# Performance work log

Measured on AMD Instinct MI355X. Metric: run time of the kernel, lower is better.

Reference implementation:

```python
import jax, jax.numpy as jnp
import numpy as np

N_NODES = 50000
N_EDGES = 800000
IN_DIM = 256
HID_DIM = 512
OUT_DIM = 256


def setup_inputs() -> dict:
    key = jax.random.key(0)
    ks = jax.random.split(key, 8)
    x = jax.random.normal(ks[0], (N_NODES, IN_DIM), dtype=jnp.float32)
    src = jax.random.randint(ks[1], (N_EDGES,), 0, N_NODES, dtype=jnp.int32)
    dst = jax.random.randint(ks[2], (N_EDGES,), 0, N_NODES, dtype=jnp.int32)
    s = 1.0 / np.sqrt(IN_DIM)
    W_self = jax.random.uniform(ks[3], (IN_DIM, HID_DIM), jnp.float32, -s, s)
    W_neigh = jax.random.uniform(ks[4], (IN_DIM, HID_DIM), jnp.float32, -s, s)
    b_enc = jnp.zeros((HID_DIM,), jnp.float32)
    s2 = 1.0 / np.sqrt(HID_DIM)
    W_dec = jax.random.uniform(ks[5], (HID_DIM, OUT_DIM), jnp.float32, -s2, s2)
    b_dec = jax.random.uniform(ks[6], (OUT_DIM,), jnp.float32, -s2, s2)
    return {"x": x, "src": src, "dst": dst, "W_self": W_self,
            "W_neigh": W_neigh, "b_enc": b_enc, "W_dec": W_dec, "b_dec": b_dec}


def reference(x, src, dst, W_self, W_neigh, b_enc, W_dec, b_dec):
    n = x.shape[0]
    # mean neighbor aggregation: scatter-sum src features onto dst, divide by in-degree
    deg = jax.ops.segment_sum(jnp.ones(dst.shape, x.dtype), dst, num_segments=n)
    neigh_sum = jax.ops.segment_sum(x[src], dst, num_segments=n)  # [N, in_dim]
    neigh_mean = neigh_sum / jnp.clip(deg, 1.0)[:, None]
    # SAGEConv 'mean': fc_self(x) + fc_neigh(h_neigh) + bias, then relu
    h = jax.nn.relu(x @ W_self + neigh_mean @ W_neigh + b_enc)  # [N, hid]
    reconstructed = h @ W_dec + b_dec  # [N, out]
    return (reconstructed, h)
```

## Files before the change

kernel.cpp:

```cpp
#include <hip/hip_runtime.h>
#include <stdint.h>

#define N_NODES 50000
#define N_EDGES 800000
#define IN_DIM 256
#define HID_DIM 512
#define OUT_DIM 256
#define SCAN_BLOCKS 196

__device__ __forceinline__ uint16_t f2b(float f) {
    uint32_t u = __builtin_bit_cast(uint32_t, f);
    uint32_t r = (u + 0x7fffu + ((u >> 16) & 1u)) >> 16;
    return (uint16_t)r;
}
__device__ __forceinline__ float b2f(uint16_t h) {
    uint32_t u = ((uint32_t)h) << 16;
    return __builtin_bit_cast(float, u);
}

__device__ __forceinline__ void async_copy16(const void* g, void* l) {
    __builtin_amdgcn_global_load_lds(
        (const __attribute__((address_space(1))) uint32_t*)g,
        (__attribute__((address_space(3))) uint32_t*)l,
        16, 0, 0);
}

typedef __bf16 bf16x8 __attribute__((ext_vector_type(8)));
typedef float f32x4 __attribute__((ext_vector_type(4)));

__global__ void k_zero_deg(uint32_t* deg) {
    int i = blockIdx.x * 256 + threadIdx.x;
    if (i < N_NODES) deg[i] = 0u;
}

__global__ void k_deg(const int* __restrict__ dst, uint32_t* __restrict__ deg) {
    int e = blockIdx.x * 256 + threadIdx.x;
    if (e < N_EDGES) atomicAdd(&deg[dst[e]], 1u);
}

__global__ void k_xcast(const float* __restrict__ x, uint16_t* __restrict__ A) {
    int id = blockIdx.x * 256 + threadIdx.x;
    if (id >= N_NODES * (IN_DIM / 4)) return;
    int row = id >> 6;
    int q = id & 63;
    float4 v = ((const float4*)x)[id];
    ushort4 o;
    o.x = f2b(v.x); o.y = f2b(v.y); o.z = f2b(v.z); o.w = f2b(v.w);
    *(ushort4*)(A + (size_t)row * 512 + q * 4) = o;
}

__global__ void k_wcat(const float* __restrict__ Ws, const float* __restrict__ Wn,
                       uint16_t* __restrict__ Wc) {
    int id = blockIdx.x * 256 + threadIdx.x;
    int n = id >> 9, k = id & 511;
    float v = (k < 256) ? Ws[(size_t)k * 512 + n] : Wn[(size_t)(k - 256) * 512 + n];
    Wc[(size_t)n * 512 + k] = f2b(v);
}

__global__ void k_wdec(const float* __restrict__ Wd, uint16_t* __restrict__ Wt) {
    int id = blockIdx.x * 256 + threadIdx.x;
    int n = id >> 9, k = id & 511;
    Wt[(size_t)n * 512 + k] = f2b(Wd[(size_t)k * 256 + n]);
}

__global__ void k_scan1(const uint32_t* __restrict__ deg, uint32_t* __restrict__ psum) {
    __shared__ uint32_t wsum[4];
    int b = blockIdx.x, t = threadIdx.x;
    int i = b * 256 + t;
    int v = (i < N_NODES) ? (int)deg[i] : 0;
#pragma unroll
    for (int o = 1; o < 64; o <<= 1) v += __shfl_xor(v, o);
    if ((t & 63) == 0) wsum[t >> 6] = (uint32_t)v;
    __syncthreads();
    if (t == 0) psum[b] = wsum[0] + wsum[1] + wsum[2] + wsum[3];
}

__global__ void k_scan2(const uint32_t* __restrict__ psum, uint32_t* __restrict__ pbase,
                        uint32_t* __restrict__ off) {
    __shared__ uint32_t sb[256];
    int t = threadIdx.x;
    uint32_t v = (t < SCAN_BLOCKS) ? psum[t] : 0u;
    sb[t] = v;
    __syncthreads();
#pragma unroll
    for (int o = 1; o < 256; o <<= 1) {
        uint32_t u = (t >= o) ? sb[t - o] : 0u;
        __syncthreads();
        sb[t] += u;
        __syncthreads();
    }
    if (t < SCAN_BLOCKS) pbase[t] = sb[t] - v;
    if (t == 0) off[N_NODES] = N_EDGES;
}

__global__ void k_scan3(const uint32_t* __restrict__ deg, const uint32_t* __restrict__ pbase,
                        uint32_t* __restrict__ off, uint32_t* __restrict__ cur) {
    __shared__ uint32_t sb[256];
    int b = blockIdx.x, t = threadIdx.x;
    int i = b * 256 + t;
    uint32_t v = (i < N_NODES) ? deg[i] : 0u;
    sb[t] = v;
    __syncthreads();
#pragma unroll
    for (int o = 1; o < 256; o <<= 1) {
        uint32_t u = (t >= o) ? sb[t - o] : 0u;
        __syncthreads();
        sb[t] += u;
        __syncthreads();
    }
    if (i < N_NODES) {
        uint32_t e = pbase[b] + sb[t] - v;
        off[i] = e;
        cur[i] = e;
    }
}

__global__ void k_scatter(const int* __restrict__ src, const int* __restrict__ dst,
                          uint32_t* __restrict__ cur, int* __restrict__ esrc) {
    int e = blockIdx.x * 256 + threadIdx.x;
    if (e >= N_EDGES) return;
    int d = dst[e];
    uint32_t pos = atomicAdd(&cur[d], 1u);
    esrc[pos] = src[e];
}

__global__ __launch_bounds__(256) void k_agg(const uint32_t* __restrict__ off,
                                             const int* __restrict__ esrc,
                                             uint16_t* __restrict__ A) {
    int node = blockIdx.x * 4 + (threadIdx.x >> 6);
    if (node >= N_NODES) return;
    int lane = threadIdx.x & 63;
    uint32_t s0 = off[node], s1 = off[node + 1];
    float a0 = 0.f, a1 = 0.f, a2 = 0.f, a3 = 0.f;
    uint32_t j = s0;
    for (; j + 4 <= s1; j += 4) {
        int sA = esrc[j], sB = esrc[j + 1], sC = esrc[j + 2], sD = esrc[j + 3];
        ushort4 v0 = *(const ushort4*)(A + (size_t)sA * 512 + lane * 4);
        ushort4 v1 = *(const ushort4*)(A + (size_t)sB * 512 + lane * 4);
        ushort4 v2 = *(const ushort4*)(A + (size_t)sC * 512 + lane * 4);
        ushort4 v3 = *(const ushort4*)(A + (size_t)sD * 512 + lane * 4);
        a0 += (b2f(v0.x) + b2f(v1.x)) + (b2f(v2.x) + b2f(v3.x));
        a1 += (b2f(v0.y) + b2f(v1.y)) + (b2f(v2.y) + b2f(v3.y));
        a2 += (b2f(v0.z) + b2f(v1.z)) + (b2f(v2.z) + b2f(v3.z));
        a3 += (b2f(v0.w) + b2f(v1.w)) + (b2f(v2.w) + b2f(v3.w));
    }
    if (j + 2 <= s1) {
        int sA = esrc[j], sB = esrc[j + 1];
        ushort4 v0 = *(const ushort4*)(A + (size_t)sA * 512 + lane * 4);
        ushort4 v1 = *(const ushort4*)(A + (size_t)sB * 512 + lane * 4);
        a0 += b2f(v0.x) + b2f(v1.x);
        a1 += b2f(v0.y) + b2f(v1.y);
        a2 += b2f(v0.z) + b2f(v1.z);
        a3 += b2f(v0.w) + b2f(v1.w);
        j += 2;
    }
    if (j < s1) {
        int sA = esrc[j];
        ushort4 v0 = *(const ushort4*)(A + (size_t)sA * 512 + lane * 4);
        a0 += b2f(v0.x); a1 += b2f(v0.y); a2 += b2f(v0.z); a3 += b2f(v0.w);
    }
    float inv = 1.0f / (float)max(s1 - s0, 1u);
    ushort4 o;
    o.x = f2b(a0 * inv); o.y = f2b(a1 * inv); o.z = f2b(a2 * inv); o.w = f2b(a3 * inv);
    *(ushort4*)(A + (size_t)node * 512 + 256 + lane * 4) = o;
}

template <int N, bool RELU, bool WBF16>
__global__ __launch_bounds__(256, 2) void k_gemm(const uint16_t* __restrict__ A,
                                                 const uint16_t* __restrict__ Bt,
                                                 const float* __restrict__ bias,
                                                 float* __restrict__ Cf,
                                                 uint16_t* __restrict__ Cb, int M) {
    constexpr int K = 512;
    constexpr int BK = 64;
    __shared__ __align__(1024) uint16_t As[128 * BK];
    __shared__ __align__(1024) uint16_t Bs[128 * BK];
    const int tid = threadIdx.x;
    const int wave = tid >> 6, lane = tid & 63;
    const int wm = wave >> 1, wn = wave & 1;
    const int m0 = blockIdx.x * 128;
    const int n0 = blockIdx.y * 128;
    const int l15 = lane & 15, l4 = lane >> 4;

    f32x4 acc[4][4] = {};

    for (int k0 = 0; k0 < K; k0 += BK) {
        __syncthreads();
#pragma unroll
        for (int j = 0; j < 4; ++j) {
            int c = j * 256 + tid;
            int row = c >> 3, p = c & 7;
            int s = p ^ (row & 7);
            int grA = min(m0 + row, M - 1);
            async_copy16(A + (size_t)grA * 512 + k0 + s * 8,
                         (char*)As + j * 4096 + wave * 1024);
            int grB = n0 + row;
            async_copy16(Bt + (size_t)grB * 512 + k0 + s * 8,
                         (char*)Bs + j * 4096 + wave * 1024);
        }
        __syncthreads();
#pragma unroll
        for (int kk = 0; kk < 2; ++kk) {
            bf16x8 af[4], bfr[4];
#pragma unroll
            for (int m = 0; m < 4; ++m) {
                int row = wm * 64 + m * 16 + l15;
                int s = (kk * 4 + l4) ^ (row & 7);
                af[m] = *(const bf16x8*)((const char*)As + row * 128 + s * 16);
            }
#pragma unroll
            for (int n = 0; n < 4; ++n) {
                int row = wn * 64 + n * 16 + l15;
                int s = (kk * 4 + l4) ^ (row & 7);
                bfr[n] = *(const bf16x8*)((const char*)Bs + row * 128 + s * 16);
            }
#pragma unroll
            for (int m = 0; m < 4; ++m)
#pragma unroll
                for (int n = 0; n < 4; ++n)
                    acc[m][n] = __builtin_amdgcn_mfma_f32_16x16x32_bf16(
                        af[m], bfr[n], acc[m][n], 0, 0, 0);
        }
    }

#pragma unroll
    for (int m = 0; m < 4; ++m) {
        int rbase = m0 + wm * 64 + m * 16 + l4 * 4;
#pragma unroll
        for (int i = 0; i < 4; ++i) {
            int r = rbase + i;
            if (r < M) {
#pragma unroll
                for (int n = 0; n < 4; ++n) {
                    int cidx = n0 + wn * 64 + n * 16 + l15;
                    float v = acc[m][n][i] + bias[cidx];
                    if (RELU) v = fmaxf(v, 0.f);
                    Cf[(size_t)r * N + cidx] = v;
                    if constexpr (WBF16) Cb[(size_t)r * N + cidx] = f2b(v);
                }
            }
        }
    }
}

extern "C" void kernel_launch(void* const* d_in, const int* in_sizes, int n_in,
                              void* d_out, int out_size, void* d_ws, size_t ws_size,
                              hipStream_t stream) {
    const float* x     = (const float*)d_in[0];
    const int*   src   = (const int*)d_in[1];
    const int*   dst   = (const int*)d_in[2];
    const float* Wself = (const float*)d_in[3];
    const float* Wneigh= (const float*)d_in[4];
    const float* benc  = (const float*)d_in[5];
    const float* Wdec  = (const float*)d_in[6];
    const float* bdec  = (const float*)d_in[7];

    float* out_recon = (float*)d_out;
    float* out_h     = (float*)d_out + (size_t)N_NODES * OUT_DIM;

    char* ws = (char*)d_ws;
    uint16_t* A    = (uint16_t*)(ws);
    uint16_t* Hb   = (uint16_t*)(ws + 51200000);
    uint16_t* Wc   = (uint16_t*)(ws + 102400000);
    uint16_t* Wd   = (uint16_t*)(ws + 102924288);
    uint32_t* deg  = (uint32_t*)(ws + 103186432);
    uint32_t* off  = (uint32_t*)(ws + 103386432);
    uint32_t* cur  = (uint32_t*)(ws + 103586560);
    int*     esrc  = (int*)(ws + 103786560);
    uint32_t* psum = (uint32_t*)(ws + 106986560);
    uint32_t* pbase= (uint32_t*)(ws + 106987344);

    k_zero_deg<<<196, 256, 0, stream>>>(deg);
    k_deg<<<3125, 256, 0, stream>>>(dst, deg);
    k_xcast<<<12500, 256, 0, stream>>>(x, A);
    k_wcat<<<1024, 256, 0, stream>>>(Wself, Wneigh, Wc);
    k_wdec<<<512, 256, 0, stream>>>(Wdec, Wd);
    k_scan1<<<SCAN_BLOCKS, 256, 0, stream>>>(deg, psum);
    k_scan2<<<1, 256, 0, stream>>>(psum, pbase, off);
    k_scan3<<<SCAN_BLOCKS, 256, 0, stream>>>(deg, pbase, off, cur);
    k_scatter<<<3125, 256, 0, stream>>>(src, dst, cur, esrc);
    k_agg<<<12500, 256, 0, stream>>>(off, esrc, A);
    k_gemm<512, true, true><<<dim3(391, 4), 256, 0, stream>>>(A, Wc, benc, out_h, Hb, N_NODES);
    k_gemm<256, false, false><<<dim3(391, 2), 256, 0, stream>>>(Hb, Wd, bdec, out_recon, nullptr, N_NODES);
}
```

Before: 269.4 us.

## Gather neighbor features in fp8, fuse prep kernels, remap GEMM blocks per XCD

Quantizes x to fp8 e4m3 alongside the bf16 cast and makes the mean aggregation gather 4-byte fp8 words instead of 8-byte bf16, halving random-gather traffic. Merges the zero/cast/weight-transpose kernels into one launch. Remaps GEMM block ids so consecutive tiles land on the same XCD for L2 reuse. Risks accuracy loss from fp8 neighbor features.

Result: faster. 236.1 us (-12.4%).

```diff
diff --git a/kernel.cpp b/kernel.cpp
--- a/kernel.cpp
+++ b/kernel.cpp
@@ -28,39 +28,91 @@
 typedef __bf16 bf16x8 __attribute__((ext_vector_type(8)));
 typedef float f32x4 __attribute__((ext_vector_type(4)));
 
-__global__ void k_zero_deg(uint32_t* deg) {
-    int i = blockIdx.x * 256 + threadIdx.x;
-    if (i < N_NODES) deg[i] = 0u;
+#if __has_builtin(__builtin_amdgcn_cvt_pk_fp8_f32) && __has_builtin(__builtin_amdgcn_cvt_pk_f32_fp8)
+#define HW_FP8 1
+#endif
+
+__device__ __forceinline__ uint8_t enc_e4m3_sw(float f) {
+    uint32_t u = __builtin_bit_cast(uint32_t, f);
+    uint32_t s = (u >> 24) & 0x80u;
+    float a = fabsf(f);
+    if (!(a > 0.f)) return (uint8_t)s;
+    if (a >= 448.f) return (uint8_t)(s | 0x7E);
+    int ebits = (int)((u >> 23) & 255u) - 127;
+    if (ebits < -6) {
+        int q = (int)rintf(a * 512.0f);
+        if (q <= 0) return (uint8_t)s;
+        if (q < 8)  return (uint8_t)(s | (uint32_t)q);
+        return (uint8_t)(s | 0x08u);
+    }
+    float scale = exp2f((float)(3 - ebits));
+    int q = (int)rintf(a * scale);
+    if (q == 16) { ebits++; q = 8; }
+    return (uint8_t)(s | (uint32_t)((ebits + 7) << 3) | (uint32_t)(q - 8));
+}
+__device__ __forceinline__ float dec_e4m3_sw(uint32_t b) {
+    uint32_t sgn = b >> 7, e = (b >> 3) & 15u, m = b & 7u;
+    float v;
+    if (e) v = __builtin_bit_cast(float, ((e + 120u) << 23) | (m << 20));
+    else   v = (float)m * 0.001953125f;
+    return sgn ? -v : v;
+}
+
+__device__ __forceinline__ uint32_t pack4_fp8(float4 v) {
+#ifdef HW_FP8
+    int w = 0;
+    w = __builtin_amdgcn_cvt_pk_fp8_f32(v.x, v.y, w, false);
+    w = __builtin_amdgcn_cvt_pk_fp8_f32(v.z, v.w, w, true);
+    return (uint32_t)w;
+#else
+    return (uint32_t)enc_e4m3_sw(v.x) | ((uint32_t)enc_e4m3_sw(v.y) << 8) |
+           ((uint32_t)enc_e4m3_sw(v.z) << 16) | ((uint32_t)enc_e4m3_sw(v.w) << 24);
+#endif
+}
+__device__ __forceinline__ void unpack4_fp8(uint32_t w, float f[4]) {
+#ifdef HW_FP8
+    auto lo = __builtin_amdgcn_cvt_pk_f32_fp8((int)w, false);
+    auto hi = __builtin_amdgcn_cvt_pk_f32_fp8((int)w, true);
+    f[0] = lo[0]; f[1] = lo[1]; f[2] = hi[0]; f[3] = hi[1];
+#else
+    f[0] = dec_e4m3_sw(w & 255u); f[1] = dec_e4m3_sw((w >> 8) & 255u);
+    f[2] = dec_e4m3_sw((w >> 16) & 255u); f[3] = dec_e4m3_sw(w >> 24);
+#endif
+}
+
+__global__ void k_prep(const float* __restrict__ x, uint16_t* __restrict__ A,
+                       uint32_t* __restrict__ Xq,
+                       const float* __restrict__ Ws, const float* __restrict__ Wn,
+                       const float* __restrict__ Wd,
+                       uint16_t* __restrict__ Wc, uint16_t* __restrict__ Wt,
+                       uint32_t* __restrict__ deg) {
+    int b = blockIdx.x, t = threadIdx.x;
+    if (b < 12500) {
+        int id = b * 256 + t;
+        int row = id >> 6, q = id & 63;
+        float4 v = ((const float4*)x)[id];
+        ushort4 o;
+        o.x = f2b(v.x); o.y = f2b(v.y); o.z = f2b(v.z); o.w = f2b(v.w);
+        *(ushort4*)(A + (size_t)row * 512 + q * 4) = o;
+        Xq[id] = pack4_fp8(v);
+    } else if (b < 12696) {
+        int i = (b - 12500) * 256 + t;
+        if (i < N_NODES) deg[i] = 0u;
+    } else if (b < 13720) {
+        int id = (b - 12696) * 256 + t;
+        int n = id >> 9, k = id & 511;
+        float v = (k < 256) ? Ws[(size_t)k * 512 + n] : Wn[(size_t)(k - 256) * 512 + n];
+        Wc[(size_t)n * 512 + k] = f2b(v);
+    } else {
+        int id = (b - 13720) * 256 + t;
+        int n = id >> 9, k = id & 511;
+        Wt[(size_t)n * 512 + k] = f2b(Wd[(size_t)k * 256 + n]);
+    }
 }
 
 __global__ void k_deg(const int* __restrict__ dst, uint32_t* __restrict__ deg) {
     int e = blockIdx.x * 256 + threadIdx.x;
     if (e < N_EDGES) atomicAdd(&deg[dst[e]], 1u);
-}
-
-__global__ void k_xcast(const float* __restrict__ x, uint16_t* __restrict__ A) {
-    int id = blockIdx.x * 256 + threadIdx.x;
-    if (id >= N_NODES * (IN_DIM / 4)) return;
-    int row = id >> 6;
-    int q = id & 63;
-    float4 v = ((const float4*)x)[id];
-    ushort4 o;
-    o.x = f2b(v.x); o.y = f2b(v.y); o.z = f2b(v.z); o.w = f2b(v.w);
-    *(ushort4*)(A + (size_t)row * 512 + q * 4) = o;
-}
-
-__global__ void k_wcat(const float* __restrict__ Ws, const float* __restrict__ Wn,
-                       uint16_t* __restrict__ Wc) {
-    int id = blockIdx.x * 256 + threadIdx.x;
-    int n = id >> 9, k = id & 511;
-    float v = (k < 256) ? Ws[(size_t)k * 512 + n] : Wn[(size_t)(k - 256) * 512 + n];
-    Wc[(size_t)n * 512 + k] = f2b(v);
-}
-
-__global__ void k_wdec(const float* __restrict__ Wd, uint16_t* __restrict__ Wt) {
-    int id = blockIdx.x * 256 + threadIdx.x;
-    int n = id >> 9, k = id & 511;
-    Wt[(size_t)n * 512 + k] = f2b(Wd[(size_t)k * 256 + n]);
 }
 
 __global__ void k_scan1(const uint32_t* __restrict__ deg, uint32_t* __restrict__ psum) {
@@ -126,6 +178,7 @@
 
 __global__ __launch_bounds__(256) void k_agg(const uint32_t* __restrict__ off,
                                              const int* __restrict__ esrc,
+                                             const uint32_t* __restrict__ Xq,
                                              uint16_t* __restrict__ A) {
     int node = blockIdx.x * 4 + (threadIdx.x >> 6);
     if (node >= N_NODES) return;
@@ -135,29 +188,24 @@
     uint32_t j = s0;
     for (; j + 4 <= s1; j += 4) {
         int sA = esrc[j], sB = esrc[j + 1], sC = esrc[j + 2], sD = esrc[j + 3];
-        ushort4 v0 = *(const ushort4*)(A + (size_t)sA * 512 + lane * 4);
-        ushort4 v1 = *(const ushort4*)(A + (size_t)sB * 512 + lane * 4);
-        ushort4 v2 = *(const ushort4*)(A + (size_t)sC * 512 + lane * 4);
-        ushort4 v3 = *(const ushort4*)(A + (size_t)sD * 512 + lane * 4);
-        a0 += (b2f(v0.x) + b2f(v1.x)) + (b2f(v2.x) + b2f(v3.x));
-        a1 += (b2f(v0.y) + b2f(v1.y)) + (b2f(v2.y) + b2f(v3.y));
-        a2 += (b2f(v0.z) + b2f(v1.z)) + (b2f(v2.z) + b2f(v3.z));
-        a3 += (b2f(v0.w) + b2f(v1.w)) + (b2f(v2.w) + b2f(v3.w));
-    }
-    if (j + 2 <= s1) {
-        int sA = esrc[j], sB = esrc[j + 1];
-        ushort4 v0 = *(const ushort4*)(A + (size_t)sA * 512 + lane * 4);
-        ushort4 v1 = *(const ushort4*)(A + (size_t)sB * 512 + lane * 4);
-        a0 += b2f(v0.x) + b2f(v1.x);
-        a1 += b2f(v0.y) + b2f(v1.y);
-        a2 += b2f(v0.z) + b2f(v1.z);
-        a3 += b2f(v0.w) + b2f(v1.w);
-        j += 2;
-    }
-    if (j < s1) {
+        uint32_t w0 = Xq[(size_t)sA * 64 + lane];
+        uint32_t w1 = Xq[(size_t)sB * 64 + lane];
+        uint32_t w2 = Xq[(size_t)sC * 64 + lane];
+        uint32_t w3 = Xq[(size_t)sD * 64 + lane];
+        float f0[4], f1[4], f2[4], f3[4];
+        unpack4_fp8(w0, f0); unpack4_fp8(w1, f1);
+        unpack4_fp8(w2, f2); unpack4_fp8(w3, f3);
+        a0 += (f0[0] + f1[0]) + (f2[0] + f3[0]);
+        a1 += (f0[1] + f1[1]) + (f2[1] + f3[1]);
+        a2 += (f0[2] + f1[2]) + (f2[2] + f3[2]);
+        a3 += (f0[3] + f1[3]) + (f2[3] + f3[3]);
+    }
+    for (; j < s1; ++j) {
         int sA = esrc[j];
-        ushort4 v0 = *(const ushort4*)(A + (size_t)sA * 512 + lane * 4);
-        a0 += b2f(v0.x); a1 += b2f(v0.y); a2 += b2f(v0.z); a3 += b2f(v0.w);
+        uint32_t w0 = Xq[(size_t)sA * 64 + lane];
+        float f0[4];
+        unpack4_fp8(w0, f0);
+        a0 += f0[0]; a1 += f0[1]; a2 += f0[2]; a3 += f0[3];
     }
     float inv = 1.0f / (float)max(s1 - s0, 1u);
     ushort4 o;
@@ -165,7 +213,7 @@
     *(ushort4*)(A + (size_t)node * 512 + 256 + lane * 4) = o;
 }
 
-template <int N, bool RELU, bool WBF16>
+template <int N, int NY, bool RELU, bool WBF16>
 __global__ __launch_bounds__(256, 2) void k_gemm(const uint16_t* __restrict__ A,
                                                  const uint16_t* __restrict__ Bt,
                                                  const float* __restrict__ bias,
@@ -178,8 +226,15 @@
     const int tid = threadIdx.x;
     const int wave = tid >> 6, lane = tid & 63;
     const int wm = wave >> 1, wn = wave & 1;
-    const int m0 = blockIdx.x * 128;
-    const int n0 = blockIdx.y * 128;
+
+    const int nwg = gridDim.x;
+    const int bid = blockIdx.x;
+    const int xcd = bid & 7, o = bid >> 3;
+    const int q = nwg >> 3, r = nwg & 7;
+    const int work = (xcd < r ? xcd * (q + 1) : r * (q + 1) + (xcd - r) * q) + o;
+    const int m0 = (work / NY) * 128;
+    const int n0 = (work % NY) * 128;
+
     const int l15 = lane & 15, l4 = lane >> 4;
 
     f32x4 acc[4][4] = {};
@@ -228,15 +283,15 @@
         int rbase = m0 + wm * 64 + m * 16 + l4 * 4;
 #pragma unroll
         for (int i = 0; i < 4; ++i) {
-            int r = rbase + i;
-            if (r < M) {
+            int r2 = rbase + i;
+            if (r2 < M) {
 #pragma unroll
                 for (int n = 0; n < 4; ++n) {
                     int cidx = n0 + wn * 64 + n * 16 + l15;
                     float v = acc[m][n][i] + bias[cidx];
                     if (RELU) v = fmaxf(v, 0.f);
-                    Cf[(size_t)r * N + cidx] = v;
-                    if constexpr (WBF16) Cb[(size_t)r * N + cidx] = f2b(v);
+                    Cf[(size_t)r2 * N + cidx] = v;
+                    if constexpr (WBF16) Cb[(size_t)r2 * N + cidx] = f2b(v);
                 }
             }
         }
@@ -269,17 +324,15 @@
     int*     esrc  = (int*)(ws + 103786560);
     uint32_t* psum = (uint32_t*)(ws + 106986560);
     uint32_t* pbase= (uint32_t*)(ws + 106987344);
-
-    k_zero_deg<<<196, 256, 0, stream>>>(deg);
+    uint32_t* Xq   = (uint32_t*)(ws + 106988544);
+
+    k_prep<<<14232, 256, 0, stream>>>(x, A, Xq, Wself, Wneigh, Wdec, Wc, Wd, deg);
     k_deg<<<3125, 256, 0, stream>>>(dst, deg);
-    k_xcast<<<12500, 256, 0, stream>>>(x, A);
-    k_wcat<<<1024, 256, 0, stream>>>(Wself, Wneigh, Wc);
-    k_wdec<<<512, 256, 0, stream>>>(Wdec, Wd);
     k_scan1<<<SCAN_BLOCKS, 256, 0, stream>>>(deg, psum);
     k_scan2<<<1, 256, 0, stream>>>(psum, pbase, off);
     k_scan3<<<SCAN_BLOCKS, 256, 0, stream>>>(deg, pbase, off, cur);
     k_scatter<<<3125, 256, 0, stream>>>(src, dst, cur, esrc);
-    k_agg<<<12500, 256, 0, stream>>>(off, esrc, A);
-    k_gemm<512, true, true><<<dim3(391, 4), 256, 0, stream>>>(A, Wc, benc, out_h, Hb, N_NODES);
-    k_gemm<256, false, false><<<dim3(391, 2), 256, 0, stream>>>(Hb, Wd, bdec, out_recon, nullptr, N_NODES);
-}
+    k_agg<<<12500, 256, 0, stream>>>(off, esrc, Xq, A);
+    k_gemm<512, 4, true, true><<<1564, 256, 0, stream>>>(A, Wc, benc, out_h, Hb, N_NODES);
+    k_gemm<256, 2, false, false><<<782, 256, 0, stream>>>(Hb, Wd, bdec, out_recon, nullptr, N_NODES);
+}
```
